# Performance work log

Hardware: AMD Instinct MI355X
Metric: run time of the kernel (lower is better)

Reference implementation:

```python
import jax, jax.numpy as jnp
import numpy as np

DIM = 1024
D_SRC = 1024
H = 16
HD = DIM // H
SCALE = 1.0 / np.sqrt(DIM)  # module uses 1/sqrt(internal_dim), not head_dim


def setup_inputs() -> dict:
    key = jax.random.key(0)
    ks = jax.random.split(key, 7)
    B, T = 2, 2048
    Q = jax.random.normal(ks[0], (B, T, DIM), dtype=jnp.float32)
    K = jax.random.normal(ks[1], (B, T, D_SRC), dtype=jnp.float32)
    V = jax.random.normal(ks[2], (B, T, D_SRC), dtype=jnp.float32)
    # torch nn.Linear weights: (out_features, in_features); y = x @ W.T
    s = 0.02
    Wq = jax.random.normal(ks[3], (DIM, DIM), dtype=jnp.float32) * s
    Wk = jax.random.normal(ks[4], (DIM, D_SRC), dtype=jnp.float32) * s
    Wv = jax.random.normal(ks[5], (DIM, D_SRC), dtype=jnp.float32) * s
    Wo = jax.random.normal(ks[6], (DIM, DIM), dtype=jnp.float32) * s
    return {"Q": Q, "K": K, "V": V, "Wq": Wq, "Wk": Wk, "Wv": Wv, "Wo": Wo}


def _split_heads(x):  # (B,T,DIM) -> (B,H,T,HD)
    B, T, _ = x.shape
    return x.reshape(B, T, H, HD).transpose(0, 2, 1, 3)


def reference(Q, K, V, Wq, Wk, Wv, Wo):
    B, T, _ = Q.shape
    q = _split_heads(Q @ Wq.T)
    k = _split_heads(K @ Wk.T)
    v = _split_heads(V @ Wv.T)
    att = jnp.einsum('bhid,bhjd->bhij', q, k) * SCALE
    causal = jnp.tril(jnp.ones((T, T), dtype=bool))
    att = jnp.where(causal[None, None], att, -jnp.inf)
    att = jax.nn.softmax(att, axis=-1)
    y = jnp.einsum('bhij,bhjd->bhid', att, v)
    y = y.transpose(0, 2, 1, 3).reshape(B, T, DIM)
    y = y @ Wo.T
    return y, att
```

## Files before the change

### kernel.cpp

```cpp
#include <hip/hip_runtime.h>
#include <hip/hip_bf16.h>

#define Bb 2
#define Tt 2048
#define DIMd 1024
#define Hh 16
#define HDh 64
#define MTOK (Bb * Tt)
#define NSCALE 0.03125f

typedef __attribute__((ext_vector_type(8))) short bf16x8;
typedef __attribute__((ext_vector_type(4))) float floatx4;

__device__ __forceinline__ unsigned short f2bf(float f) {
    union { float f; unsigned int u; } a; a.f = f;
    const unsigned int u = a.u;
    return (unsigned short)((u + 0x7FFFu + ((u >> 16) & 1u)) >> 16);
}

__device__ __forceinline__ void gl_lds16(const void* g, void* l) {
    __builtin_amdgcn_global_load_lds((const __attribute__((address_space(1))) void*)g,
                                     (__attribute__((address_space(3))) void*)l, 16, 0, 0);
}

__global__ __launch_bounds__(256) void cvt_all(
    const float* __restrict__ s0, const float* __restrict__ s1, const float* __restrict__ s2,
    const float* __restrict__ s3, const float* __restrict__ s4, const float* __restrict__ s5,
    const float* __restrict__ s6,
    unsigned short* __restrict__ d0, unsigned short* __restrict__ d1, unsigned short* __restrict__ d2,
    unsigned short* __restrict__ d3, unsigned short* __restrict__ d4, unsigned short* __restrict__ d5,
    unsigned short* __restrict__ d6) {
    const int blk = blockIdx.x;
    const float* src; unsigned short* dst; int rb;
    if (blk < 12288) {
        const int r = blk >> 12;
        rb  = blk & 4095;
        src = (r == 0) ? s0 : ((r == 1) ? s1 : s2);
        dst = (r == 0) ? d0 : ((r == 1) ? d1 : d2);
    } else {
        const int r = (blk - 12288) >> 10;
        rb  = blk & 1023;
        src = (r == 0) ? s3 : ((r == 1) ? s4 : ((r == 2) ? s5 : s6));
        dst = (r == 0) ? d3 : ((r == 1) ? d4 : ((r == 2) ? d5 : d6));
    }
    const int i = (rb * 256 + threadIdx.x) * 4;
    const float4 v = *(const float4*)(src + i);
    ushort4 o;
    o.x = f2bf(v.x); o.y = f2bf(v.y); o.z = f2bf(v.z); o.w = f2bf(v.w);
    *(ushort4*)(dst + i) = o;
}

template <int BF16OUT>
__global__ __launch_bounds__(256) void gemm_bt_mfma(const unsigned short* __restrict__ A,
                                                    const unsigned short* __restrict__ W,
                                                    void* __restrict__ Cv,
                                                    int M, int N, int K) {
    __shared__ unsigned short As[128 * 32];
    __shared__ unsigned short Bs[128 * 32];

    const int tid  = threadIdx.x;
    const int wave = tid >> 6;
    const int lane = tid & 63;
    const int m0 = blockIdx.y * 128;
    const int n0 = blockIdx.x * 128;
    const int wm = (wave >> 1) * 64;
    const int wn = (wave & 1) * 64;
    const int qd = lane >> 4;
    const int ln16 = lane & 15;

    floatx4 acc[4][4];
#pragma unroll
    for (int mi = 0; mi < 4; ++mi)
#pragma unroll
        for (int ni = 0; ni < 4; ++ni) acc[mi][ni] = (floatx4){0.f, 0.f, 0.f, 0.f};

    for (int k0 = 0; k0 < K; k0 += 32) {
#pragma unroll
        for (int t = 0; t < 2; ++t) {
            const int c = t * 256 + wave * 64 + lane;
            const int row = c >> 2;
            const int col = (c & 3) * 8;
            gl_lds16(A + (size_t)(m0 + row) * K + k0 + col, &As[c * 8]);
            gl_lds16(W + (size_t)(n0 + row) * K + k0 + col, &Bs[c * 8]);
        }
        __syncthreads();

        bf16x8 af[4], bfr[4];
#pragma unroll
        for (int mi = 0; mi < 4; ++mi)
            af[mi] = *(const bf16x8*)&As[(wm + mi * 16 + ln16) * 32 + qd * 8];
#pragma unroll
        for (int ni = 0; ni < 4; ++ni)
            bfr[ni] = *(const bf16x8*)&Bs[(wn + ni * 16 + ln16) * 32 + qd * 8];
#pragma unroll
        for (int mi = 0; mi < 4; ++mi)
#pragma unroll
            for (int ni = 0; ni < 4; ++ni)
                acc[mi][ni] = __builtin_amdgcn_mfma_f32_16x16x32_bf16(af[mi], bfr[ni], acc[mi][ni], 0, 0, 0);
        __syncthreads();
    }

#pragma unroll
    for (int mi = 0; mi < 4; ++mi)
#pragma unroll
        for (int ni = 0; ni < 4; ++ni) {
            const int gn = n0 + wn + ni * 16 + ln16;
#pragma unroll
            for (int r = 0; r < 4; ++r) {
                const int gm = m0 + wm + mi * 16 + qd * 4 + r;
                if (BF16OUT)
                    ((unsigned short*)Cv)[(size_t)gm * N + gn] = f2bf(acc[mi][ni][r]);
                else
                    ((float*)Cv)[(size_t)gm * N + gn] = acc[mi][ni][r];
            }
        }
}

#define PSTR 72

__global__ __launch_bounds__(256) void fused_attn(const unsigned short* __restrict__ qp,
                                                  const unsigned short* __restrict__ kp,
                                                  const unsigned short* __restrict__ vt,
                                                  float* __restrict__ att,
                                                  unsigned short* __restrict__ ymid,
                                                  float* __restrict__ lws) {
    __shared__ unsigned short Ks[64 * 64];
    __shared__ unsigned short Vs[64 * 64];
    __shared__ unsigned short Ps[64 * PSTR];

    const int bid = blockIdx.x;
    const int bh  = bid & 31;
    const int it  = 31 - (bid >> 5);
    const int h   = bh & (Hh - 1);
    const int b   = bh >> 4;
    const int tid  = threadIdx.x;
    const int w    = tid >> 6;
    const int lane = tid & 63;
    const int qd   = lane >> 4;
    const int ln16 = lane & 15;
    const int i0   = it * 64;
    const int ig   = i0 + w * 16 + ln16;

    bf16x8 qf[2];
    {
        const unsigned short* qrow = qp + (size_t)(b * Tt + ig) * DIMd + h * HDh;
        qf[0] = *(const bf16x8*)(qrow + qd * 8);
        qf[1] = *(const bf16x8*)(qrow + 32 + qd * 8);
    }

    floatx4 oacc[4];
#pragma unroll
    for (int dt = 0; dt < 4; ++dt) oacc[dt] = (floatx4){0.f, 0.f, 0.f, 0.f};
    float lsum = 0.f;

    unsigned short* Pw = &Ps[w * 16 * PSTR];
    float* arow = att + ((size_t)bh * Tt + ig) * Tt;

    for (int jt = 0; jt <= it; ++jt) {
        const int j0 = jt * 64;
        __syncthreads();

#pragma unroll
        for (int t = 0; t < 2; ++t) {
            const int c   = w * 128 + t * 64 + lane;
            const int row = c >> 3;
            const int cb  = c & 7;
            const int col8 = ((cb ^ (row & 7)) * 8);
            gl_lds16(kp + (size_t)(b * Tt + j0 + row) * DIMd + h * HDh + col8, &Ks[c * 8]);
            gl_lds16(vt + (size_t)(h * HDh + row) * MTOK + b * Tt + j0 + col8, &Vs[c * 8]);
        }
        __syncthreads();

        floatx4 sacc[4];
#pragma unroll
        for (int ct = 0; ct < 4; ++ct) sacc[ct] = (floatx4){0.f, 0.f, 0.f, 0.f};
        __builtin_amdgcn_s_setprio(1);
#pragma unroll
        for (int ks = 0; ks < 2; ++ks)
#pragma unroll
            for (int ct = 0; ct < 4; ++ct) {
                const int row = ct * 16 + ln16;
                const bf16x8 kf = *(const bf16x8*)&Ks[row * 64 + (((ks * 4 + qd) ^ (row & 7)) * 8)];
                sacc[ct] = __builtin_amdgcn_mfma_f32_16x16x32_bf16(kf, qf[ks], sacc[ct], 0, 0, 0);
            }
        __builtin_amdgcn_s_setprio(0);

        float rs = 0.f;
#pragma unroll
        for (int ct = 0; ct < 4; ++ct) {
            const int jb = j0 + ct * 16 + qd * 4;
            float4 ev;
            {
                const float e0 = (jb + 0 <= ig) ? __expf(sacc[ct][0] * NSCALE) : 0.f;
                const float e1 = (jb + 1 <= ig) ? __expf(sacc[ct][1] * NSCALE) : 0.f;
                const float e2 = (jb + 2 <= ig) ? __expf(sacc[ct][2] * NSCALE) : 0.f;
                const float e3 = (jb + 3 <= ig) ? __expf(sacc[ct][3] * NSCALE) : 0.f;
                ev = make_float4(e0, e1, e2, e3);
                rs += e0 + e1 + e2 + e3;
            }
            *(float4*)(arow + jb) = ev;
            ushort4 pk;
            pk.x = f2bf(ev.x); pk.y = f2bf(ev.y); pk.z = f2bf(ev.z); pk.w = f2bf(ev.w);
            *(ushort4*)&Pw[ln16 * PSTR + ct * 16 + qd * 4] = pk;
        }
        rs += __shfl_xor(rs, 16);
        rs += __shfl_xor(rs, 32);
        lsum += rs;

        __builtin_amdgcn_s_setprio(1);
#pragma unroll
        for (int ks = 0; ks < 2; ++ks) {
            const bf16x8 pf = *(const bf16x8*)&Pw[ln16 * PSTR + ks * 32 + qd * 8];
#pragma unroll
            for (int dt = 0; dt < 4; ++dt) {
                const int row = dt * 16 + ln16;
                const bf16x8 vf = *(const bf16x8*)&Vs[row * 64 + (((ks * 4 + qd) ^ (row & 7)) * 8)];
                oacc[dt] = __builtin_amdgcn_mfma_f32_16x16x32_bf16(pf, vf, oacc[dt], 0, 0, 0);
            }
        }
        __builtin_amdgcn_s_setprio(0);
    }

    float lssrc[4];
#pragma unroll
    for (int r = 0; r < 4; ++r) lssrc[r] = __shfl(lsum, qd * 4 + r);
#pragma unroll
    for (int r = 0; r < 4; ++r) {
        const float inv = 1.f / lssrc[r];
        unsigned short* yr = ymid + (size_t)(b * Tt + i0 + w * 16 + qd * 4 + r) * DIMd + h * HDh + ln16;
#pragma unroll
        for (int dt = 0; dt < 4; ++dt)
            yr[dt * 16] = f2bf(oacc[dt][r] * inv);
    }
    if (qd == 0) lws[(size_t)bh * Tt + ig] = lsum;
}

__global__ __launch_bounds__(256) void att_rescale(float* __restrict__ att,
                                                   const float* __restrict__ lws) {
    const int row = blockIdx.x;
    const int i   = row & (Tt - 1);
    const float inv = 1.f / lws[row];
    float4* arow = (float4*)(att + (size_t)row * Tt);
    const int tid = threadIdx.x;
#pragma unroll
    for (int q = 0; q < 2; ++q) {
        const int f4 = tid + q * 256;
        const int j  = f4 * 4;
        float4 v;
        if (j <= i) {
            v = arow[f4];
            v.x = (j + 0 <= i) ? v.x * inv : 0.f;
            v.y = (j + 1 <= i) ? v.y * inv : 0.f;
            v.z = (j + 2 <= i) ? v.z * inv : 0.f;
            v.w = (j + 3 <= i) ? v.w * inv : 0.f;
        } else {
            v = make_float4(0.f, 0.f, 0.f, 0.f);
        }
        arow[f4] = v;
    }
}

extern "C" void kernel_launch(void* const* d_in, const int* in_sizes, int n_in,
                              void* d_out, int out_size, void* d_ws, size_t ws_size,
                              hipStream_t stream) {
    const float* Q  = (const float*)d_in[0];
    const float* K  = (const float*)d_in[1];
    const float* V  = (const float*)d_in[2];
    const float* Wq = (const float*)d_in[3];
    const float* Wk = (const float*)d_in[4];
    const float* Wv = (const float*)d_in[5];
    const float* Wo = (const float*)d_in[6];

    const size_t nytok = (size_t)Bb * Tt * DIMd;
    const size_t nw    = (size_t)DIMd * DIMd;
    float* y   = (float*)d_out;
    float* att = y + nytok;

    char* w = (char*)d_ws;
    unsigned short* qp  = (unsigned short*)w;    w += nytok * 2;
    unsigned short* kp  = (unsigned short*)w;    w += nytok * 2;
    unsigned short* vt  = (unsigned short*)w;    w += nytok * 2;
    unsigned short* Qb  = (unsigned short*)w;    w += nytok * 2;
    unsigned short* Kb  = (unsigned short*)w;    w += nytok * 2;
    unsigned short* Vb  = (unsigned short*)w;    w += nytok * 2;
    unsigned short* Wqb = (unsigned short*)w;    w += nw * 2;
    unsigned short* Wkb = (unsigned short*)w;    w += nw * 2;
    unsigned short* Wvb = (unsigned short*)w;    w += nw * 2;
    unsigned short* Wob = (unsigned short*)w;    w += nw * 2;
    float* lws = (float*)w;
    unsigned short* ymid_b = Qb;

    const int M = Bb * Tt;

    cvt_all<<<16384, 256, 0, stream>>>(Q, K, V, Wq, Wk, Wv, Wo,
                                       Qb, Kb, Vb, Wqb, Wkb, Wvb, Wob);

    dim3 gg(DIMd / 128, M / 128);
    gemm_bt_mfma<1><<<gg, 256, 0, stream>>>(Qb, Wqb, qp, M, DIMd, DIMd);
    gemm_bt_mfma<1><<<gg, 256, 0, stream>>>(Kb, Wkb, kp, M, DIMd, DIMd);
    dim3 ggv(M / 128, DIMd / 128);
    gemm_bt_mfma<1><<<ggv, 256, 0, stream>>>(Wvb, Vb, vt, DIMd, M, DIMd);

    fused_attn<<<32 * 32, 256, 0, stream>>>(qp, kp, vt, att, ymid_b, lws);
    att_rescale<<<Bb * Hh * Tt, 256, 0, stream>>>(att, lws);

    gemm_bt_mfma<0><<<gg, 256, 0, stream>>>(ymid_b, Wob, y, M, DIMd, DIMd);
}
```

Baseline: 830.6 us.

## Merge QKV GEMMs into one launch, fuse out-proj with att rescale, swizzle LDS

Runs the three projection GEMMs as a single 768-block launch and folds the attention-row rescale into the output-projection launch as extra blocks, so the two can overlap on the GPU. The GEMM tile now uses a K-step of 64 with an XOR-swizzled LDS layout, meant to avoid bank conflicts and halve the number of barriers, and raises wave priority around the MFMA block. The costs are doubled LDS per block, which may lower occupancy, and a heterogeneous grid where GEMM and bandwidth-bound rescale blocks compete for the same resources.

```diff
diff --git a/kernel.cpp b/kernel.cpp
--- a/kernel.cpp
+++ b/kernel.cpp
@@ -51,22 +51,19 @@
 }
 
 template <int BF16OUT>
-__global__ __launch_bounds__(256) void gemm_bt_mfma(const unsigned short* __restrict__ A,
-                                                    const unsigned short* __restrict__ W,
-                                                    void* __restrict__ Cv,
-                                                    int M, int N, int K) {
-    __shared__ unsigned short As[128 * 32];
-    __shared__ unsigned short Bs[128 * 32];
-
+__device__ __forceinline__ void gemm_tile(unsigned short* As, unsigned short* Bs,
+                                          const unsigned short* __restrict__ A,
+                                          const unsigned short* __restrict__ W,
+                                          void* __restrict__ Cv,
+                                          int N, int K, int m0, int n0) {
     const int tid  = threadIdx.x;
     const int wave = tid >> 6;
     const int lane = tid & 63;
-    const int m0 = blockIdx.y * 128;
-    const int n0 = blockIdx.x * 128;
     const int wm = (wave >> 1) * 64;
     const int wn = (wave & 1) * 64;
     const int qd = lane >> 4;
     const int ln16 = lane & 15;
+    const int x7 = ln16 & 7;
 
     floatx4 acc[4][4];
 #pragma unroll
@@ -74,29 +71,34 @@
 #pragma unroll
         for (int ni = 0; ni < 4; ++ni) acc[mi][ni] = (floatx4){0.f, 0.f, 0.f, 0.f};
 
-    for (int k0 = 0; k0 < K; k0 += 32) {
-#pragma unroll
-        for (int t = 0; t < 2; ++t) {
-            const int c = t * 256 + wave * 64 + lane;
-            const int row = c >> 2;
-            const int col = (c & 3) * 8;
+    for (int k0 = 0; k0 < K; k0 += 64) {
+#pragma unroll
+        for (int t = 0; t < 4; ++t) {
+            const int c   = t * 256 + wave * 64 + lane;
+            const int row = c >> 3;
+            const int col = ((c & 7) ^ (row & 7)) * 8;
             gl_lds16(A + (size_t)(m0 + row) * K + k0 + col, &As[c * 8]);
             gl_lds16(W + (size_t)(n0 + row) * K + k0 + col, &Bs[c * 8]);
         }
         __syncthreads();
 
-        bf16x8 af[4], bfr[4];
-#pragma unroll
-        for (int mi = 0; mi < 4; ++mi)
-            af[mi] = *(const bf16x8*)&As[(wm + mi * 16 + ln16) * 32 + qd * 8];
-#pragma unroll
-        for (int ni = 0; ni < 4; ++ni)
-            bfr[ni] = *(const bf16x8*)&Bs[(wn + ni * 16 + ln16) * 32 + qd * 8];
-#pragma unroll
-        for (int mi = 0; mi < 4; ++mi)
+#pragma unroll
+        for (int ks = 0; ks < 2; ++ks) {
+            bf16x8 af[4], bfr[4];
+#pragma unroll
+            for (int mi = 0; mi < 4; ++mi)
+                af[mi] = *(const bf16x8*)&As[(wm + mi * 16 + ln16) * 64 + (((ks * 4 + qd) ^ x7) * 8)];
 #pragma unroll
             for (int ni = 0; ni < 4; ++ni)
-                acc[mi][ni] = __builtin_amdgcn_mfma_f32_16x16x32_bf16(af[mi], bfr[ni], acc[mi][ni], 0, 0, 0);
+                bfr[ni] = *(const bf16x8*)&Bs[(wn + ni * 16 + ln16) * 64 + (((ks * 4 + qd) ^ x7) * 8)];
+            __builtin_amdgcn_s_setprio(1);
+#pragma unroll
+            for (int mi = 0; mi < 4; ++mi)
+#pragma unroll
+                for (int ni = 0; ni < 4; ++ni)
+                    acc[mi][ni] = __builtin_amdgcn_mfma_f32_16x16x32_bf16(af[mi], bfr[ni], acc[mi][ni], 0, 0, 0);
+            __builtin_amdgcn_s_setprio(0);
+        }
         __syncthreads();
     }
 
@@ -114,6 +116,63 @@
                     ((float*)Cv)[(size_t)gm * N + gn] = acc[mi][ni][r];
             }
         }
+}
+
+__global__ __launch_bounds__(256) void gemm_proj3(
+    const unsigned short* __restrict__ Qb, const unsigned short* __restrict__ Wqb, unsigned short* __restrict__ qp,
+    const unsigned short* __restrict__ Kb, const unsigned short* __restrict__ Wkb, unsigned short* __restrict__ kp,
+    const unsigned short* __restrict__ Vb, const unsigned short* __restrict__ Wvb, unsigned short* __restrict__ vt) {
+    __shared__ unsigned short As[128 * 64];
+    __shared__ unsigned short Bs[128 * 64];
+    const int bid = blockIdx.x;
+    if (bid < 256) {
+        gemm_tile<1>(As, Bs, Qb, Wqb, qp, DIMd, DIMd, (bid >> 3) * 128, (bid & 7) * 128);
+    } else if (bid < 512) {
+        const int r = bid - 256;
+        gemm_tile<1>(As, Bs, Kb, Wkb, kp, DIMd, DIMd, (r >> 3) * 128, (r & 7) * 128);
+    } else {
+        const int r = bid - 512;
+        gemm_tile<1>(As, Bs, Wvb, Vb, vt, MTOK, DIMd, (r >> 5) * 128, (r & 31) * 128);
+    }
+}
+
+__global__ __launch_bounds__(256) void gemm_o_rescale(const unsigned short* __restrict__ ymid,
+                                                      const unsigned short* __restrict__ Wob,
+                                                      float* __restrict__ y,
+                                                      float* __restrict__ att,
+                                                      const float* __restrict__ lws) {
+    __shared__ unsigned short As[128 * 64];
+    __shared__ unsigned short Bs[128 * 64];
+    const int bid = blockIdx.x;
+    if (bid < 256) {
+        gemm_tile<0>(As, Bs, ymid, Wob, y, DIMd, DIMd, (bid >> 3) * 128, (bid & 7) * 128);
+        return;
+    }
+    const int rb  = bid - 256;
+    const int tid = threadIdx.x;
+#pragma unroll
+    for (int rr = 0; rr < 16; ++rr) {
+        const int row = rb * 16 + rr;
+        const int i   = row & (Tt - 1);
+        const float inv = 1.f / lws[row];
+        float4* arow = (float4*)(att + (size_t)row * Tt);
+#pragma unroll
+        for (int q = 0; q < 2; ++q) {
+            const int f4 = tid + q * 256;
+            const int j  = f4 * 4;
+            float4 v;
+            if (j <= i) {
+                v = arow[f4];
+                v.x = (j + 0 <= i) ? v.x * inv : 0.f;
+                v.y = (j + 1 <= i) ? v.y * inv : 0.f;
+                v.z = (j + 2 <= i) ? v.z * inv : 0.f;
+                v.w = (j + 3 <= i) ? v.w * inv : 0.f;
+            } else {
+                v = make_float4(0.f, 0.f, 0.f, 0.f);
+            }
+            arow[f4] = v;
+        }
+    }
 }
 
 #define PSTR 72
@@ -233,31 +292,6 @@
             yr[dt * 16] = f2bf(oacc[dt][r] * inv);
     }
     if (qd == 0) lws[(size_t)bh * Tt + ig] = lsum;
-}
-
-__global__ __launch_bounds__(256) void att_rescale(float* __restrict__ att,
-                                                   const float* __restrict__ lws) {
-    const int row = blockIdx.x;
-    const int i   = row & (Tt - 1);
-    const float inv = 1.f / lws[row];
-    float4* arow = (float4*)(att + (size_t)row * Tt);
-    const int tid = threadIdx.x;
-#pragma unroll
-    for (int q = 0; q < 2; ++q) {
-        const int f4 = tid + q * 256;
-        const int j  = f4 * 4;
-        float4 v;
-        if (j <= i) {
-            v = arow[f4];
-            v.x = (j + 0 <= i) ? v.x * inv : 0.f;
-            v.y = (j + 1 <= i) ? v.y * inv : 0.f;
-            v.z = (j + 2 <= i) ? v.z * inv : 0.f;
-            v.w = (j + 3 <= i) ? v.w * inv : 0.f;
-        } else {
-            v = make_float4(0.f, 0.f, 0.f, 0.f);
-        }
-        arow[f4] = v;
-    }
 }
 
 extern "C" void kernel_launch(void* const* d_in, const int* in_sizes, int n_in,
@@ -290,19 +324,12 @@
     float* lws = (float*)w;
     unsigned short* ymid_b = Qb;
 
-    const int M = Bb * Tt;
-
     cvt_all<<<16384, 256, 0, stream>>>(Q, K, V, Wq, Wk, Wv, Wo,
                                        Qb, Kb, Vb, Wqb, Wkb, Wvb, Wob);
 
-    dim3 gg(DIMd / 128, M / 128);
-    gemm_bt_mfma<1><<<gg, 256, 0, stream>>>(Qb, Wqb, qp, M, DIMd, DIMd);
-    gemm_bt_mfma<1><<<gg, 256, 0, stream>>>(Kb, Wkb, kp, M, DIMd, DIMd);
-    dim3 ggv(M / 128, DIMd / 128);
-    gemm_bt_mfma<1><<<ggv, 256, 0, stream>>>(Wvb, Vb, vt, DIMd, M, DIMd);
+    gemm_proj3<<<768, 256, 0, stream>>>(Qb, Wqb, qp, Kb, Wkb, kp, Vb, Wvb, vt);
 
     fused_attn<<<32 * 32, 256, 0, stream>>>(qp, kp, vt, att, ymid_b, lws);
-    att_rescale<<<Bb * Hh * Tt, 256, 0, stream>>>(att, lws);
-
-    gemm_bt_mfma<0><<<gg, 256, 0, stream>>>(ymid_b, Wob, y, M, DIMd, DIMd);
-}
+
+    gemm_o_rescale<<<256 + 4096, 256, 0, stream>>>(ymid_b, Wob, y, att, lws);
+}
```

Result: slower. 848.7 us (+2.2%).
